# Performance work log

Measured on AMD Instinct MI355X. Metric: run time of the kernel, lower is better.

The kernel has to match this reference:

```python
import jax, jax.numpy as jnp
import numpy as np


def conv1d(x, w, b):
    # x: (N, Cin, W), w: (Cout, Cin, K) -> (N, Cout, W-K+1), VALID conv (torch Conv1d)
    y = jax.lax.conv_general_dilated(x, w, (1,), 'VALID', dimension_numbers=('NCH', 'OIH', 'NCH'))
    return y + b[None, :, None]


def cnn_block(x, w, b):
    # conv1d then MaxPool1d over the full valid length -> (N, Cout)
    return jnp.max(conv1d(x, w, b), axis=2)


def highway(x, Wp, bp, Wg, bg):
    p = jax.nn.relu(x @ Wp.T + bp)
    g = jax.nn.sigmoid(x @ Wg.T + bg)
    return g * p + (1.0 - g) * x


def lstm_masked(x, lens, Wih, Whh, bih, bhh):
    # x: (N, Wt, E); lens: (N,) valid lengths. Emulates pack_padded_sequence +
    # nn.LSTM + pad_packed_sequence: outputs are h_t for t < len, zeros after.
    N, Wt, _ = x.shape
    H = Whh.shape[1]
    bias = bih + bhh
    h0 = jnp.zeros((N, H), x.dtype)

    def step(carry, inp):
        xt, t = inp
        h, c = carry
        z = xt @ Wih.T + h @ Whh.T + bias  # (N, 4H), gate order i,f,g,o
        i, f, g, o = jnp.split(z, 4, axis=-1)
        c2 = jax.nn.sigmoid(f) * c + jax.nn.sigmoid(i) * jnp.tanh(g)
        h2 = jax.nn.sigmoid(o) * jnp.tanh(c2)
        valid = (t < lens)[:, None]
        h2 = jnp.where(valid, h2, h)
        c2 = jnp.where(valid, c2, c)
        return (h2, c2), jnp.where(valid, h2, jnp.zeros_like(h2))

    xs = jnp.moveaxis(x, 1, 0)  # (Wt, N, E)
    ts = jnp.arange(Wt)
    _, out = jax.lax.scan(step, (h0, h0), (xs, ts))
    return jnp.moveaxis(out, 0, 1)  # (N, Wt, H)


def setup_inputs() -> dict:
    key = jax.random.key(0)
    ks = jax.random.split(key, 32)
    B, T = 32, 48
    WL, WA, WE = 33, 50, 30
    EL, EA, EE, H = 300, 988, 20, 128
    CL, CA, CE = 128, 256, 64
    s = 0.02
    inp = {
        'x_lin': jax.random.normal(ks[0], (B, T, WL, EL), jnp.float32),
        'x_aco': jax.random.normal(ks[1], (B, T, WA, EA), jnp.float32),
        'x_emo': jax.random.normal(ks[2], (B, T, WE, EE), jnp.float32),
        'window_length': jax.random.randint(ks[3], (B, T), 0, WE).astype(jnp.int32) + 1,
        'length': jax.random.randint(ks[4], (B,), 1, T + 1).astype(jnp.int32),
        # CNN params
        'convL_w': s * jax.random.normal(ks[5], (CL, EL, 5), jnp.float32),
        'convL_b': jnp.zeros((CL,), jnp.float32),
        'convA_w': s * jax.random.normal(ks[6], (CA, EA, 10), jnp.float32),
        'convA_b': jnp.zeros((CA,), jnp.float32),
        'convE_w': s * jax.random.normal(ks[7], (CE, H, 3), jnp.float32),
        'convE_b': jnp.zeros((CE,), jnp.float32),
        # Highway params
        'hwL_Wp': s * jax.random.normal(ks[8], (CL, CL), jnp.float32),
        'hwL_bp': jnp.zeros((CL,), jnp.float32),
        'hwL_Wg': s * jax.random.normal(ks[9], (CL, CL), jnp.float32),
        'hwL_bg': jnp.zeros((CL,), jnp.float32),
        'hwA_Wp': s * jax.random.normal(ks[10], (CA, CA), jnp.float32),
        'hwA_bp': jnp.zeros((CA,), jnp.float32),
        'hwA_Wg': s * jax.random.normal(ks[11], (CA, CA), jnp.float32),
        'hwA_bg': jnp.zeros((CA,), jnp.float32),
        'hwE_Wp': s * jax.random.normal(ks[12], (CE, CE), jnp.float32),
        'hwE_bp': jnp.zeros((CE,), jnp.float32),
        'hwE_Wg': s * jax.random.normal(ks[13], (CE, CE), jnp.float32),
        'hwE_bg': jnp.zeros((CE,), jnp.float32),
        # LSTM params (nn.LSTM, 1 layer, batch_first)
        'lstm_Wih': s * jax.random.normal(ks[14], (4 * H, EE), jnp.float32),
        'lstm_Whh': s * jax.random.normal(ks[15], (4 * H, H), jnp.float32),
        'lstm_bih': jnp.zeros((4 * H,), jnp.float32),
        'lstm_bhh': jnp.zeros((4 * H,), jnp.float32),
    }
    return inp


def reference(x_lin, x_aco, x_emo, window_length, length,
              convL_w, convL_b, convA_w, convA_b, convE_w, convE_b,
              hwL_Wp, hwL_bp, hwL_Wg, hwL_bg,
              hwA_Wp, hwA_bp, hwA_Wg, hwA_bg,
              hwE_Wp, hwE_bp, hwE_Wg, hwE_bg,
              lstm_Wih, lstm_Whh, lstm_bih, lstm_bhh):
    B, T = x_lin.shape[:2]
    # Linguistic: per-window CNN + Highway (dropout = identity in eval)
    xl = x_lin.reshape(B * T, x_lin.shape[2], x_lin.shape[3]).transpose(0, 2, 1)  # (BT, 300, WL)
    outL = highway(cnn_block(xl, convL_w, convL_b), hwL_Wp, hwL_bp, hwL_Wg, hwL_bg)
    outL = outL.reshape(B, T, -1)
    # Acoustic
    xa = x_aco.reshape(B * T, x_aco.shape[2], x_aco.shape[3]).transpose(0, 2, 1)  # (BT, 988, WA)
    outA = highway(cnn_block(xa, convA_w, convA_b), hwA_Wp, hwA_bp, hwA_Wg, hwA_bg)
    outA = outA.reshape(B, T, -1)
    # Emotient: ragged per-window LSTM (packed semantics) -> CNN -> Highway
    xe = x_emo.reshape(B * T, x_emo.shape[2], x_emo.shape[3])  # (BT, WE, 20)
    lens = window_length.reshape(B * T)
    h = lstm_masked(xe, lens, lstm_Wih, lstm_Whh, lstm_bih, lstm_bhh)  # (BT, WE, 128)
    outE = highway(cnn_block(h.transpose(0, 2, 1), convE_w, convE_b), hwE_Wp, hwE_bp, hwE_Wg, hwE_bg)
    outE = outE.reshape(B, T, -1)
    # Concatenate modalities -> (B, T, 128+256+64) fed to the downstream head
    return jnp.concatenate([outL, outA, outE], axis=2)
```

## Files before the change

### kernel.cpp

```cpp
#include <hip/hip_runtime.h>
#include <hip/hip_bf16.h>
#include <math.h>

#define BTOT 1536
#define EL 300
#define ELP 320
#define WL_ 33
#define CL 128
#define LOUTL 29
#define KPL 1600
#define EA 988
#define EAP 992
#define WA_ 50
#define CA 256
#define LOUTA 41
#define KPA 9920
#define EE 20
#define WE_ 30
#define HH 128
#define CE 64
#define LOUTE 28
#define KPE 384
#define KDIML 1500
#define KDIMA 9880
#define KDIME 384

typedef __attribute__((ext_vector_type(4))) float f32x4;
typedef __attribute__((ext_vector_type(8))) short short8;

__device__ __forceinline__ unsigned short f2bf(float f) {
    unsigned int x = __float_as_uint(f);
    unsigned int r = (x + 0x7fffu + ((x >> 16) & 1u)) >> 16;
    return (unsigned short)r;
}

__device__ __forceinline__ float sigmf(float x) {
    return __builtin_amdgcn_rcpf(1.f + __expf(-x));
}
__device__ __forceinline__ float tanh_fast(float x) {
    return 1.f - 2.f * __builtin_amdgcn_rcpf(1.f + __expf(2.f * x));
}

#define GLD16(gp, lp) __builtin_amdgcn_global_load_lds( \
    (const __attribute__((address_space(1))) void*)(gp), \
    (__attribute__((address_space(3))) void*)(lp), 16, 0, 0)

template<int N> __device__ __forceinline__ void vmwait() {
    if constexpr (N == 0) asm volatile("s_waitcnt vmcnt(0)" ::: "memory");
    else if constexpr (N == 1) asm volatile("s_waitcnt vmcnt(1)" ::: "memory");
    else if constexpr (N == 2) asm volatile("s_waitcnt vmcnt(2)" ::: "memory");
    else if constexpr (N == 3) asm volatile("s_waitcnt vmcnt(3)" ::: "memory");
    else if constexpr (N == 4) asm volatile("s_waitcnt vmcnt(4)" ::: "memory");
    else if constexpr (N == 5) asm volatile("s_waitcnt vmcnt(5)" ::: "memory");
    else if constexpr (N == 6) asm volatile("s_waitcnt vmcnt(6)" ::: "memory");
    else if constexpr (N == 8) asm volatile("s_waitcnt vmcnt(8)" ::: "memory");
    else static_assert(N == 0, "add case");
}

__device__ __forceinline__ void tr_one(const float* a, float* at, int R, int C, int idx) {
    int r = idx / C, c = idx - r * C;
    at[c * R + r] = a[idx];
}
template<int CIN, int CINP, int KW, int COUT, int KPAD>
__device__ __forceinline__ void wt_one(const float* w, unsigned short* wt, int idx) {
    int co = idx / KPAD;
    int p  = idx - co * KPAD;
    int k  = p / CINP;
    int c  = p - k * CINP;
    float v = 0.f;
    if (k < KW && c < CIN) v = w[(co * CIN + c) * KW + k];
    wt[idx] = f2bf(v);
}
template<bool BIG>
__global__ void prep_all(const float* hwL_Wp, float* WpTL, const float* hwL_Wg, float* WgTL,
                         const float* hwA_Wp, float* WpTA, const float* hwA_Wg, float* WgTA,
                         const float* hwE_Wp, float* WpTE, const float* hwE_Wg, float* WgTE,
                         const float* lstm_Wih, float* WihT, const float* lstm_Whh, float* WhhT,
                         const float* convL_w, unsigned short* wtL,
                         const float* convE_w, unsigned short* wtE,
                         const float* convA_w, unsigned short* wtA,
                         unsigned short* whh_bf, unsigned short* wihp_bf) {
    constexpr int S1 = 16384, S2 = 16384, S3 = 65536, S4 = 65536, S5 = 4096, S6 = 4096;
    constexpr int S7 = 512 * 20, S8 = 512 * 128;
    constexpr int S9 = 128 * KPL, S10 = 64 * KPE, S11 = 512 * 128, S12 = 512 * 32;
    constexpr int S13 = CA * KPA;
    constexpr int SMALL = S1 + S2 + S3 + S4 + S5 + S6 + S7 + S8;
    constexpr int TOTAL = BIG ? (SMALL + S9 + S10 + S11 + S12 + S13) : SMALL;
    int stride = gridDim.x * blockDim.x;
    for (int i = blockIdx.x * blockDim.x + threadIdx.x; i < TOTAL; i += stride) {
        int idx = i;
        if (idx < S1) { tr_one(hwL_Wp, WpTL, 128, 128, idx); continue; } idx -= S1;
        if (idx < S2) { tr_one(hwL_Wg, WgTL, 128, 128, idx); continue; } idx -= S2;
        if (idx < S3) { tr_one(hwA_Wp, WpTA, 256, 256, idx); continue; } idx -= S3;
        if (idx < S4) { tr_one(hwA_Wg, WgTA, 256, 256, idx); continue; } idx -= S4;
        if (idx < S5) { tr_one(hwE_Wp, WpTE, 64, 64, idx); continue; } idx -= S5;
        if (idx < S6) { tr_one(hwE_Wg, WgTE, 64, 64, idx); continue; } idx -= S6;
        if (idx < S7) { tr_one(lstm_Wih, WihT, 512, 20, idx); continue; } idx -= S7;
        if (idx < S8) { tr_one(lstm_Whh, WhhT, 512, 128, idx); continue; } idx -= S8;
        if constexpr (BIG) {
            if (idx < S9) { wt_one<EL, ELP, 5, CL, KPL>(convL_w, wtL, idx); continue; } idx -= S9;
            if (idx < S10) { wt_one<HH, HH, 3, CE, KPE>(convE_w, wtE, idx); continue; } idx -= S10;
            if (idx < S11) { whh_bf[idx] = f2bf(lstm_Whh[idx]); continue; } idx -= S11;
            if (idx < S12) { int col = idx >> 5, e = idx & 31;
                             wihp_bf[idx] = (e < 20) ? f2bf(lstm_Wih[col * 20 + e]) : (unsigned short)0;
                             continue; } idx -= S12;
            wt_one<EA, EAP, 10, CA, KPA>(convA_w, wtA, idx);
        }
    }
}

template<int CIN, int CINP>
__device__ __forceinline__ void cvt_chunk(const float* in, unsigned short* out, int idx) {
    constexpr int CH = CINP / 8;
    int row = idx / CH, c0 = (idx - row * CH) * 8;
    const float* src = in + (size_t)row * CIN + c0;
    union { short8 s; unsigned short u[8]; } o;
    if (c0 + 8 <= CIN) {
        float4 v0 = *(const float4*)src;
        float4 v1 = *(const float4*)(src + 4);
        o.u[0]=f2bf(v0.x); o.u[1]=f2bf(v0.y); o.u[2]=f2bf(v0.z); o.u[3]=f2bf(v0.w);
        o.u[4]=f2bf(v1.x); o.u[5]=f2bf(v1.y); o.u[6]=f2bf(v1.z); o.u[7]=f2bf(v1.w);
    } else {
        #pragma unroll
        for (int j = 0; j < 8; ++j) o.u[j] = (c0 + j < CIN) ? f2bf(src[j]) : (unsigned short)0;
    }
    *(short8*)(out + (size_t)row * CINP + c0) = o.s;
}

#define LSTM_BLOCKS 96
#define CVTA_BLOCKS 1440

__global__ __launch_bounds__(512, 1)
void lstm_cvt(const float* __restrict__ x_emo,
              const unsigned short* __restrict__ wihp_bf, const unsigned short* __restrict__ whh_bf,
              const float* __restrict__ bih, const float* __restrict__ bhh,
              const int* __restrict__ lens, unsigned short* __restrict__ hbuf,
              const float* __restrict__ xa, unsigned short* __restrict__ outa)
{
    __shared__ __align__(16) unsigned short xq[WE_ * 16 * 32];
    __shared__ __align__(16) char h_s[2 * 16 * HH * 2];

    if (blockIdx.x >= LSTM_BLOCKS) {
        constexpr int NAC = (BTOT * WA_) * (EAP / 8);
        int stride = CVTA_BLOCKS * 512;
        for (int i = (blockIdx.x - LSTM_BLOCKS) * 512 + threadIdx.x; i < NAC; i += stride)
            cvt_chunk<EA, EAP>(xa, outa, i);
        return;
    }

    const int tid  = threadIdx.x;
    const int w    = tid >> 6;
    const int lane = tid & 63;
    const int lr   = lane & 15;
    const int lq   = lane >> 4;
    const int s0   = blockIdx.x * 16;
    const int c    = w * 16 + lr;

    short8 bfr[4][4];
    short8 bw[4];
    float bj[4];
    #pragma unroll
    for (int g = 0; g < 4; ++g) {
        int col = g * 128 + c;
        #pragma unroll
        for (int kt = 0; kt < 4; ++kt)
            bfr[g][kt] = *(const short8*)(whh_bf + (size_t)col * 128 + kt * 32 + lq * 8);
        bw[g] = *(const short8*)(wihp_bf + (size_t)col * 32 + lq * 8);
        bj[g] = bih[col] + bhh[col];
    }
    int len4[4];
    #pragma unroll
    for (int j = 0; j < 4; ++j) len4[j] = lens[s0 + lq * 4 + j];

    for (int i = tid; i < WE_ * 16 * 32; i += 512) {
        int t = i >> 9, r = (i >> 5) & 15, e = i & 31;
        xq[i] = (e < 20) ? f2bf(x_emo[(((size_t)(s0 + r) * WE_) + t) * 20 + e]) : (unsigned short)0;
    }
    for (int i = tid; i < 2048; i += 512) ((unsigned int*)h_s)[i] = 0u;

    float c_prev[4] = {0.f, 0.f, 0.f, 0.f};
    unsigned short hb_prev[4] = {0, 0, 0, 0};
    __syncthreads();

    for (int t = 0; t < WE_; ++t) {
        const char* hsr = h_s + (t & 1) * 4096;
        char* hsw = h_s + ((t & 1) ^ 1) * 4096;
        short8 ax = *(const short8*)((const char*)xq + (size_t)(t * 16 + lr) * 64 + lq * 16);
        short8 af[4];
        #pragma unroll
        for (int kt = 0; kt < 4; ++kt)
            af[kt] = *(const short8*)(hsr + ((lr * 256 + kt * 64 + lq * 16) ^ ((lr & 7) << 4)));
        f32x4 acc[4];
        #pragma unroll
        for (int g = 0; g < 4; ++g)
            acc[g] = __builtin_amdgcn_mfma_f32_16x16x32_bf16(ax, bw[g], (f32x4){0.f,0.f,0.f,0.f}, 0, 0, 0);
        #pragma unroll
        for (int kt = 0; kt < 4; ++kt)
            #pragma unroll
            for (int g = 0; g < 4; ++g)
                acc[g] = __builtin_amdgcn_mfma_f32_16x16x32_bf16(af[kt], bfr[g][kt], acc[g], 0, 0, 0);
        #pragma unroll
        for (int j = 0; j < 4; ++j) {
            int s = lq * 4 + j;
            float zi = acc[0][j] + bj[0];
            float zf = acc[1][j] + bj[1];
            float zg = acc[2][j] + bj[2];
            float zo = acc[3][j] + bj[3];
            float si = sigmf(zi), sf = sigmf(zf), so = sigmf(zo);
            float tg = tanh_fast(zg);
            float c2 = sf * c_prev[j] + si * tg;
            float h2 = so * tanh_fast(c2);
            bool valid = (t < len4[j]);
            c_prev[j] = valid ? c2 : c_prev[j];
            unsigned short h2b = f2bf(h2);
            unsigned short hn = valid ? h2b : hb_prev[j];
            hb_prev[j] = hn;
            *(unsigned short*)(hsw + (((s * HH + c) * 2) ^ ((s & 7) << 4))) = hn;
            hbuf[(((size_t)(s0 + s) * WE_) + t) * HH + c] = valid ? h2b : (unsigned short)0;
        }
        __syncthreads();
    }
}

#define CONVA_BLOCKS 768
#define CVTL_BLOCKS 512
__global__ __launch_bounds__(256, 2)
void conv_a_v11(const unsigned short* __restrict__ xb, const unsigned short* __restrict__ wt,
                const float* __restrict__ bias, float* __restrict__ pooled,
                const float* __restrict__ xl, unsigned short* __restrict__ outl)
{
    constexpr int LOUT = LOUTA, WIN = WA_, CINP = EAP, BN = 128, COUT = CA;
    constexpr int CCH  = CINP / 32;
    constexpr int KB   = CINP * 2;
    constexpr int KTOTB = CINP * 10 * 2;
    constexpr int ABUF = 4 * 64 * 64;
    constexpr int BBUF = BN * 64;
    constexpr int CPQ  = 96;

    __shared__ __align__(16) char smem[2 * ABUF + 5 * BBUF];

    if (blockIdx.x >= CONVA_BLOCKS) {
        constexpr int NLC = (BTOT * WL_) * (ELP / 8);
        int stride = CVTL_BLOCKS * 256;
        for (int i = (blockIdx.x - CONVA_BLOCKS) * 256 + threadIdx.x; i < NLC; i += stride)
            cvt_chunk<EL, ELP>(xl, outl, i);
        return;
    }

    const int tid  = threadIdx.x;
    const int lane = tid & 63;
    const int wid  = tid >> 6;
    const int lr   = lane & 15;
    const int lq   = lane >> 4;
    const int lq16 = lq * 16;

    int xcd = blockIdx.x & 7;
    int n = xcd & 1;
    int m = (xcd >> 1) * CPQ + (blockIdx.x >> 3);

    f32x4 acc[3][8];
    #pragma unroll
    for (int i = 0; i < 3; ++i)
        #pragma unroll
        for (int j = 0; j < 8; ++j) acc[i][j] = (f32x4){0.f, 0.f, 0.f, 0.f};

    const int aw_r = tid >> 2;
    const int aw   = (aw_r < WIN) ? aw_r : (WIN - 1);
    const int slot = tid & 3;
    const char* asrc[4];
    #pragma unroll
    for (int i = 0; i < 4; ++i)
        asrc[i] = (const char*)xb + ((size_t)((m * 4 + i) * WIN + aw)) * KB
                + ((slot * 16) ^ (((aw_r >> 1) & 3) << 4));
    const char* bsrc[2];
    #pragma unroll
    for (int i = 0; i < 2; ++i) {
        int col = (tid + i * 256) >> 2;
        bsrc[i] = (const char*)wt + (size_t)(n * BN + col) * KTOTB
                + ((slot * 16) ^ (((col >> 1) & 3) << 4));
    }

    char* const abuf0 = smem;
    char* const abuf1 = smem + ABUF;
    char* const bbase = smem + 2 * ABUF;

    int cbo[8];
    #pragma unroll
    for (int nf = 0; nf < 8; ++nf) {
        int cb = nf * 16 + lr;
        cbo[nf] = cb * 64 + (lq16 ^ (((cb >> 1) & 3) << 4));
    }

    #pragma unroll
    for (int i = 0; i < 4; ++i)
        GLD16(asrc[i], abuf0 + i * 4096 + tid * 16);
    #pragma unroll
    for (int s = 0; s < 3; ++s) {
        GLD16(bsrc[0] + s * KB, bbase + s * BBUF + tid * 16);
        GLD16(bsrc[1] + s * KB, bbase + s * BBUF + 4096 + tid * 16);
    }
    vmwait<0>();
    __builtin_amdgcn_s_barrier();

    int bcur = 0;

#define VSTEP(KK, DOA, DOBAR, WN, DOBSTG, CHN) do {                                \
    const char* bb = bbase + bcur * BBUF;                                          \
    short8 afr[3];                                                                 \
    _Pragma("unroll")                                                              \
    for (int o = 0; o < 3; ++o) {                                                  \
        int row = o * 16 + lr + (KK);                                              \
        afr[o] = *(const short8*)(awave + row * 64 + (lq16 ^ (((row >> 1) & 3) << 4))); \
    }                                                                              \
    short8 bf[8];                                                                  \
    _Pragma("unroll")                                                              \
    for (int nf = 0; nf < 8; ++nf) bf[nf] = *(const short8*)(bb + cbo[nf]);        \
    if (DOBSTG) {                                                                  \
        constexpr int K3 = ((KK) + 3 < 10) ? (KK) + 3 : (KK) - 7;                  \
        int boff = K3 * KB + (CHN) * 64;                                           \
        int b3 = bcur + 3; if (b3 >= 5) b3 -= 5;                                   \
        char* bstg = bbase + b3 * BBUF;                                            \
        GLD16(bsrc[0] + boff, bstg + tid * 16);                                    \
        GLD16(bsrc[1] + boff, bstg + 4096 + tid * 16);                             \
    }                                                                              \
    if (DOA) GLD16(asrc[(KK) - 5] + (size_t)(ci + 1) * 64,                         \
                   abn + ((KK) - 5) * 4096 + tid * 16);                            \
    __builtin_amdgcn_s_setprio(1);                                                 \
    _Pragma("unroll")                                                              \
    for (int nf = 0; nf < 8; ++nf)                                                 \
        _Pragma("unroll")                                                          \
        for (int o = 0; o < 3; ++o)                                                \
            acc[o][nf] = __builtin_amdgcn_mfma_f32_16x16x32_bf16(afr[o], bf[nf], acc[o][nf], 0, 0, 0); \
    __builtin_amdgcn_s_setprio(0);                                                 \
    if (DOBAR) { vmwait<WN>(); asm volatile("" ::: "memory");                      \
                 __builtin_amdgcn_s_barrier(); }                                   \
    bcur = (bcur == 4) ? 0 : bcur + 1;                                             \
} while (0)

    for (int ci = 0; ci < CCH - 1; ++ci) {
        const char* ab = (ci & 1) ? abuf1 : abuf0;
        char* abn = (ci & 1) ? abuf0 : abuf1;
        const char* awave = ab + wid * 4096;
        VSTEP(0, false, false, 0, true, ci);
        VSTEP(1, false, true,  2, true, ci);
        VSTEP(2, false, false, 0, true, ci);
        VSTEP(3, false, true,  2, true, ci);
        VSTEP(4, false, false, 0, true, ci);
        VSTEP(5, true,  true,  3, true, ci);
        VSTEP(6, true,  false, 0, true, ci);
        VSTEP(7, true,  true,  3, true, ci + 1);
        VSTEP(8, true,  false, 0, true, ci + 1);
        VSTEP(9, false, true,  2, true, ci + 1);
    }
    {
        const int ci = CCH - 1;
        const char* ab = (ci & 1) ? abuf1 : abuf0;
        char* abn = (ci & 1) ? abuf0 : abuf1; (void)abn;
        const char* awave = ab + wid * 4096;
        VSTEP(0, false, false, 0, true,  ci);
        VSTEP(1, false, true,  2, true,  ci);
        VSTEP(2, false, false, 0, true,  ci);
        VSTEP(3, false, true,  2, true,  ci);
        VSTEP(4, false, false, 0, true,  ci);
        VSTEP(5, false, true,  2, true,  ci);
        VSTEP(6, false, false, 0, true,  ci);
        VSTEP(7, false, true,  0, false, ci);
        VSTEP(8, false, false, 0, false, ci);
        VSTEP(9, false, true,  0, false, ci);
    }
#undef VSTEP

    const int bt = m * 4 + wid;
    #pragma unroll
    for (int nf = 0; nf < 8; ++nf) {
        float mx = -INFINITY;
        #pragma unroll
        for (int o = 0; o < 3; ++o) {
            int rb = o * 16 + lq * 4;
            #pragma unroll
            for (int j = 0; j < 4; ++j)
                if (rb + j < LOUT) mx = fmaxf(mx, acc[o][nf][j]);
        }
        mx = fmaxf(mx, __shfl_xor(mx, 16, 64));
        mx = fmaxf(mx, __shfl_xor(mx, 32, 64));
        if (lane < 16) {
            int col = n * BN + nf * 16 + lane;
            pooled[(size_t)bt * COUT + col] = mx + bias[col];
        }
    }
}

template<int LOUT, int WIN, int CINP, int KW, int BN, int NS, int MFR, int COUT>
__global__ __launch_bounds__(256, 2)
void conv_pool_v10(const unsigned short* __restrict__ xb, const unsigned short* __restrict__ wt,
                   const float* __restrict__ bias, float* __restrict__ pooled)
{
    constexpr int CCH   = CINP / 32;
    constexpr int KB    = CINP * 2;
    constexpr int KTOTB = CINP * KW * 2;
    constexpr int NFR   = BN / 16;
    constexpr int B_IT  = BN / 64;
    constexpr int ABUF  = 4 * 64 * 64;
    constexpr int BBUF  = BN * 64;
    constexpr int CPQ   = (BTOT / 4) / 4;

    __shared__ __align__(16) char smem[2 * ABUF + 4 * BBUF];

    const int tid  = threadIdx.x;
    const int lane = tid & 63;
    const int wid  = tid >> 6;
    const int lr   = lane & 15;
    const int lq   = lane >> 4;
    const int lq16 = lq * 16;

    int m, n;
    if constexpr (NS == 2) {
        int xcd = blockIdx.x & 7;
        n = xcd & 1;
        m = (xcd >> 1) * CPQ + (blockIdx.x >> 3);
    } else {
        m = blockIdx.x; n = 0;
    }

    f32x4 acc[MFR][NFR];
    #pragma unroll
    for (int i = 0; i < MFR; ++i)
        #pragma unroll
        for (int j = 0; j < NFR; ++j) acc[i][j] = (f32x4){0.f, 0.f, 0.f, 0.f};

    const int aw_r = tid >> 2;
    const int aw   = (aw_r < WIN) ? aw_r : (WIN - 1);
    const int slot = tid & 3;
    const char* asrc[4];
    #pragma unroll
    for (int i = 0; i < 4; ++i)
        asrc[i] = (const char*)xb + ((size_t)((m * 4 + i) * WIN + aw)) * KB
                + ((slot * 16) ^ (((aw_r >> 1) & 3) << 4));
    const char* bsrc[B_IT];
    #pragma unroll
    for (int i = 0; i < B_IT; ++i) {
        int col = (tid + i * 256) >> 2;
        bsrc[i] = (const char*)wt + (size_t)(n * BN + col) * KTOTB
                + ((slot * 16) ^ (((col >> 1) & 3) << 4));
    }

    char* const abuf0 = smem;
    char* const abuf1 = smem + ABUF;
    char* const bbase = smem + 2 * ABUF;

    int cbo[NFR];
    #pragma unroll
    for (int nf = 0; nf < NFR; ++nf) {
        int cb = nf * 16 + lr;
        cbo[nf] = cb * 64 + (lq16 ^ (((cb >> 1) & 3) << 4));
    }

    #pragma unroll
    for (int i = 0; i < 4; ++i)
        GLD16(asrc[i], abuf0 + i * 4096 + tid * 16);
    #pragma unroll
    for (int s = 0; s < 3; ++s)
        #pragma unroll
        for (int i = 0; i < B_IT; ++i)
            GLD16(bsrc[i] + s * KB, bbase + s * BBUF + i * 4096 + tid * 16);
    vmwait<0>();
    __builtin_amdgcn_s_barrier();

    int bcur = 0;

#define STEP(KK, WN, TAIL) do {                                                    \
    const char* bb = bbase + bcur * BBUF;                                          \
    short8 afr[MFR];                                                               \
    _Pragma("unroll")                                                              \
    for (int o = 0; o < MFR; ++o) {                                                \
        int row = o * 16 + lr + (KK);                                              \
        afr[o] = *(const short8*)(awave + row * 64 + (lq16 ^ (((row >> 1) & 3) << 4))); \
    }                                                                              \
    short8 bf[NFR];                                                                \
    _Pragma("unroll")                                                              \
    for (int nf = 0; nf < NFR; ++nf) bf[nf] = *(const short8*)(bb + cbo[nf]);      \
    if (!(TAIL) || (KK) < KW - 3) {                                                \
        constexpr int k3_ = ((KK) + 3 < KW) ? (KK) + 3 : (KK) + 3 - KW;            \
        int boff = k3_ * KB + (((KK) + 3 < KW) ? ci : ci + 1) * 64;                \
        char* bstg = bbase + ((bcur + 3) & 3) * BBUF;                              \
        _Pragma("unroll")                                                          \
        for (int i = 0; i < B_IT; ++i)                                             \
            GLD16(bsrc[i] + boff, bstg + i * 4096 + tid * 16);                     \
    }                                                                              \
    if (!(TAIL)) {                                                                 \
        if (KW >= 8) {                                                             \
            if ((KK) < 4)                                                          \
                GLD16(asrc[(KK) & 3] + (size_t)(ci + 1) * 64, abn + ((KK) & 3) * 4096 + tid * 16); \
        } else if ((KK) == 0) {                                                    \
            _Pragma("unroll")                                                      \
            for (int i = 0; i < 4; ++i)                                            \
                GLD16(asrc[i] + (size_t)(ci + 1) * 64, abn + i * 4096 + tid * 16); \
        }                                                                          \
    }                                                                              \
    __builtin_amdgcn_s_setprio(1);                                                 \
    _Pragma("unroll")                                                              \
    for (int nf = 0; nf < NFR; ++nf)                                               \
        _Pragma("unroll")                                                          \
        for (int o = 0; o < MFR; ++o)                                              \
            acc[o][nf] = __builtin_amdgcn_mfma_f32_16x16x32_bf16(afr[o], bf[nf], acc[o][nf], 0, 0, 0); \
    __builtin_amdgcn_s_setprio(0);                                                 \
    vmwait<WN>();                                                                  \
    asm volatile("" ::: "memory");                                                 \
    __builtin_amdgcn_s_barrier();                                                  \
    bcur = (bcur + 1) & 3;                                                         \
} while (0)

    for (int ci = 0; ci < CCH - 1; ++ci) {
        const char* ab = (ci & 1) ? abuf1 : abuf0;
        char* abn = (ci & 1) ? abuf0 : abuf1;
        const char* awave = ab + wid * 4096;
        if constexpr (KW == 5) {
            STEP(0, 8, false); STEP(1, 8, false); STEP(2, 4, false); STEP(3, 4, false); STEP(4, 4, false);
        } else {
            STEP(0, 6, false); STEP(1, 6, false); STEP(2, 2, false);
        }
    }
    {
        const int ci = CCH - 1;
        const char* ab = (ci & 1) ? abuf1 : abuf0;
        char* abn = (ci & 1) ? abuf0 : abuf1; (void)abn;
        const char* awave = ab + wid * 4096;
        if constexpr (KW == 5) {
            STEP(0, 4, true); STEP(1, 4, true); STEP(2, 2, true); STEP(3, 0, true); STEP(4, 0, true);
        } else {
            STEP(0, 1, true); STEP(1, 0, true); STEP(2, 0, true);
        }
    }
#undef STEP

    const int bt = m * 4 + wid;
    #pragma unroll
    for (int nf = 0; nf < NFR; ++nf) {
        float mx = -INFINITY;
        #pragma unroll
        for (int o = 0; o < MFR; ++o) {
            int rb = o * 16 + lq * 4;
            #pragma unroll
            for (int j = 0; j < 4; ++j)
                if (rb + j < LOUT) mx = fmaxf(mx, acc[o][nf][j]);
        }
        mx = fmaxf(mx, __shfl_xor(mx, 16, 64));
        mx = fmaxf(mx, __shfl_xor(mx, 32, 64));
        if (lane < 16) {
            int col = n * BN + nf * 16 + lane;
            pooled[(size_t)bt * COUT + col] = mx + bias[col];
        }
    }
}

#define HWA_BLOCKS 192
#define HWL_BLOCKS 96
#define HWE_BLOCKS 48
__global__ __launch_bounds__(256)
void highway_v2(const float* __restrict__ pL, const float* __restrict__ pA, const float* __restrict__ pE,
                const float* __restrict__ WpTL, const float* __restrict__ bpL,
                const float* __restrict__ WgTL, const float* __restrict__ bgL,
                const float* __restrict__ WpTA, const float* __restrict__ bpA,
                const float* __restrict__ WgTA, const float* __restrict__ bgA,
                const float* __restrict__ WpTE, const float* __restrict__ bpE,
                const float* __restrict__ WgTE, const float* __restrict__ bgE,
                float* __restrict__ out) {
    __shared__ float xs[2048];
    int bx = blockIdx.x;
    int tid = threadIdx.x;
    if (bx < HWA_BLOCKS) {
        int bt0 = bx * 8;
        #pragma unroll
        for (int s = 0; s < 8; ++s) xs[s * 256 + tid] = pA[(size_t)(bt0 + s) * 256 + tid];
        __syncthreads();
        float p[8], g[8];
        #pragma unroll
        for (int s = 0; s < 8; ++s) { p[s] = bpA[tid]; g[s] = bgA[tid]; }
        for (int c = 0; c < 256; ++c) {
            float wp = WpTA[c * 256 + tid], wg = WgTA[c * 256 + tid];
            #pragma unroll
            for (int s = 0; s < 8; ++s) {
                float xv = xs[s * 256 + c];
                p[s] += xv * wp; g[s] += xv * wg;
            }
        }
        #pragma unroll
        for (int s = 0; s < 8; ++s) {
            float pp = fmaxf(p[s], 0.f);
            float gg = sigmf(g[s]);
            out[(size_t)(bt0 + s) * 448 + 128 + tid] = gg * pp + (1.f - gg) * xs[s * 256 + tid];
        }
    } else if (bx < HWA_BLOCKS + HWL_BLOCKS) {
        int bt0 = (bx - HWA_BLOCKS) * 16;
        for (int i = tid; i < 16 * 128; i += 256) xs[i] = pL[(size_t)bt0 * 128 + i];
        __syncthreads();
        int j = tid & 127, h = tid >> 7;
        float p[8], g[8];
        #pragma unroll
        for (int s = 0; s < 8; ++s) { p[s] = bpL[j]; g[s] = bgL[j]; }
        for (int c = 0; c < 128; ++c) {
            float wp = WpTL[c * 128 + j], wg = WgTL[c * 128 + j];
            #pragma unroll
            for (int s = 0; s < 8; ++s) {
                float xv = xs[(h * 8 + s) * 128 + c];
                p[s] += xv * wp; g[s] += xv * wg;
            }
        }
        #pragma unroll
        for (int s = 0; s < 8; ++s) {
            float pp = fmaxf(p[s], 0.f);
            float gg = sigmf(g[s]);
            out[(size_t)(bt0 + h * 8 + s) * 448 + j] = gg * pp + (1.f - gg) * xs[(h * 8 + s) * 128 + j];
        }
    } else {
        int bt0 = (bx - HWA_BLOCKS - HWL_BLOCKS) * 32;
        for (int i = tid; i < 32 * 64; i += 256) xs[i] = pE[(size_t)bt0 * 64 + i];
        __syncthreads();
        int j = tid & 63, grp = tid >> 6;
        float p[8], g[8];
        #pragma unroll
        for (int s = 0; s < 8; ++s) { p[s] = bpE[j]; g[s] = bgE[j]; }
        for (int c = 0; c < 64; ++c) {
            float wp = WpTE[c * 64 + j], wg = WgTE[c * 64 + j];
            #pragma unroll
            for (int s = 0; s < 8; ++s) {
                float xv = xs[(grp * 8 + s) * 64 + c];
                p[s] += xv * wp; g[s] += xv * wg;
            }
        }
        #pragma unroll
        for (int s = 0; s < 8; ++s) {
            float pp = fmaxf(p[s], 0.f);
            float gg = sigmf(g[s]);
            out[(size_t)(bt0 + grp * 8 + s) * 448 + 384 + j] = gg * pp + (1.f - gg) * xs[(grp * 8 + s) * 64 + j];
        }
    }
}

__global__ __launch_bounds__(512)
void lstm_kernel_f32(const float* __restrict__ x, const int* __restrict__ lens,
                     const float* __restrict__ WihT, const float* __restrict__ WhhT,
                     const float* __restrict__ bih, const float* __restrict__ bhh,
                     float* __restrict__ hout) {
    int bt = blockIdx.x;
    int j  = threadIdx.x;
    __shared__ float xs[WE_][EE];
    __shared__ __align__(16) float hs[HH];
    __shared__ float zs[512];
    for (int idx = j; idx < WE_ * EE; idx += 512)
        ((float*)xs)[idx] = x[(size_t)bt * WE_ * EE + idx];
    if (j < HH) hs[j] = 0.f;
    float wih[EE];
    #pragma unroll
    for (int e = 0; e < EE; ++e) wih[e] = WihT[e * 512 + j];
    float whh[HH];
    #pragma unroll
    for (int h = 0; h < HH; ++h) whh[h] = WhhT[h * 512 + j];
    float bjv = bih[j] + bhh[j];
    float c_reg = 0.f;
    int len = lens[bt];
    __syncthreads();
    for (int t = 0; t < WE_; ++t) {
        float z = bjv;
        #pragma unroll
        for (int e = 0; e < EE; ++e) z += wih[e] * xs[t][e];
        const float4* h4 = (const float4*)hs;
        #pragma unroll
        for (int q = 0; q < HH / 4; ++q) {
            float4 hv = h4[q];
            z += whh[4*q+0] * hv.x + whh[4*q+1] * hv.y
               + whh[4*q+2] * hv.z + whh[4*q+3] * hv.w;
        }
        zs[j] = z;
        __syncthreads();
        if (j < HH) {
            float zi = zs[j], zf = zs[HH + j], zg = zs[2*HH + j], zo = zs[3*HH + j];
            float si = 1.f / (1.f + expf(-zi));
            float sf = 1.f / (1.f + expf(-zf));
            float so = 1.f / (1.f + expf(-zo));
            float tg = tanhf(zg);
            float c2 = sf * c_reg + si * tg;
            float h2 = so * tanhf(c2);
            bool valid = (t < len);
            float hn = valid ? h2 : hs[j];
            c_reg    = valid ? c2 : c_reg;
            hout[((size_t)bt * WE_ + t) * HH + j] = valid ? h2 : 0.f;
            hs[j] = hn;
        }
        __syncthreads();
    }
}

template<int CIN, int WIN, int COUT, int KDIM, int LOUT>
__global__ __launch_bounds__(256)
void conv_pool_simple(const float* __restrict__ x, const float* __restrict__ w,
                      const float* __restrict__ bias, float* __restrict__ pooled)
{
    constexpr int KW = KDIM / CIN;
    int bt = blockIdx.x;
    int co = blockIdx.y * 64 + (threadIdx.x & 63);
    int seg = threadIdx.x >> 6;
    __shared__ float part[4][64];
    float m = -INFINITY;
    for (int l = seg; l < LOUT; l += 4) {
        float acc = 0.f;
        for (int k = 0; k < KW; ++k) {
            const float* xr = x + ((size_t)bt * WIN + l + k) * CIN;
            const float* wr = w + ((size_t)co * CIN) * KW + k;
            for (int cc = 0; cc < CIN; ++cc) acc += xr[cc] * wr[(size_t)cc * KW];
        }
        m = fmaxf(m, acc);
    }
    part[seg][threadIdx.x & 63] = m;
    __syncthreads();
    if (threadIdx.x < 64) {
        float mm = fmaxf(fmaxf(part[0][threadIdx.x], part[1][threadIdx.x]),
                         fmaxf(part[2][threadIdx.x], part[3][threadIdx.x]));
        pooled[(size_t)bt * COUT + co] = mm + bias[co];
    }
}

static inline int cdiv(int a, int b) { return (a + b - 1) / b; }

extern "C" void kernel_launch(void* const* d_in, const int* in_sizes, int n_in,
                              void* d_out, int out_size, void* d_ws, size_t ws_size,
                              hipStream_t stream) {
    const float* x_lin  = (const float*)d_in[0];
    const float* x_aco  = (const float*)d_in[1];
    const float* x_emo  = (const float*)d_in[2];
    const int*   wlen   = (const int*)  d_in[3];
    const float* convL_w = (const float*)d_in[5];
    const float* convL_b = (const float*)d_in[6];
    const float* convA_w = (const float*)d_in[7];
    const float* convA_b = (const float*)d_in[8];
    const float* convE_w = (const float*)d_in[9];
    const float* convE_b = (const float*)d_in[10];
    const float* hwL_Wp = (const float*)d_in[11];
    const float* hwL_bp = (const float*)d_in[12];
    const float* hwL_Wg = (const float*)d_in[13];
    const float* hwL_bg = (const float*)d_in[14];
    const float* hwA_Wp = (const float*)d_in[15];
    const float* hwA_bp = (const float*)d_in[16];
    const float* hwA_Wg = (const float*)d_in[17];
    const float* hwA_bg = (const float*)d_in[18];
    const float* hwE_Wp = (const float*)d_in[19];
    const float* hwE_bp = (const float*)d_in[20];
    const float* hwE_Wg = (const float*)d_in[21];
    const float* hwE_bg = (const float*)d_in[22];
    const float* lstm_Wih = (const float*)d_in[23];
    const float* lstm_Whh = (const float*)d_in[24];
    const float* lstm_bih = (const float*)d_in[25];
    const float* lstm_bhh = (const float*)d_in[26];
    float* out = (float*)d_out;

    char* p0 = (char*)d_ws;
    char* p = p0;
    auto alloc = [&](size_t bytes) { char* r = p; p += (bytes + 255) & ~(size_t)255; return r; };
    float* WpTL = (float*)alloc((size_t)CL * CL * 4);
    float* WgTL = (float*)alloc((size_t)CL * CL * 4);
    float* WpTA = (float*)alloc((size_t)CA * CA * 4);
    float* WgTA = (float*)alloc((size_t)CA * CA * 4);
    float* WpTE = (float*)alloc((size_t)CE * CE * 4);
    float* WgTE = (float*)alloc((size_t)CE * CE * 4);
    float* WihT = (float*)alloc((size_t)EE * 512 * 4);
    float* WhhT = (float*)alloc((size_t)HH * 512 * 4);
    unsigned short* whh_bf  = (unsigned short*)alloc((size_t)512 * 128 * 2);
    unsigned short* wihp_bf = (unsigned short*)alloc((size_t)512 * 32 * 2);
    void*  hbuf = (void*)alloc((size_t)BTOT * WE_ * HH * 4);
    float* pL   = (float*)alloc((size_t)BTOT * CL * 4);
    float* pA   = (float*)alloc((size_t)BTOT * CA * 4);
    float* pE   = (float*)alloc((size_t)BTOT * CE * 4);
    unsigned short* wtA = (unsigned short*)alloc((size_t)CA * KPA * 2);
    unsigned short* wtL = (unsigned short*)alloc((size_t)CL * KPL * 2);
    unsigned short* wtE = (unsigned short*)alloc((size_t)CE * KPE * 2);
    unsigned short* xlin_p = (unsigned short*)alloc((size_t)BTOT * WL_ * ELP * 2 + 64);
    unsigned short* xaco_p = (unsigned short*)alloc((size_t)BTOT * WA_ * EAP * 2 + 64);
    size_t need = (size_t)(p - p0);
    bool big = ws_size >= need;

    if (big) {
        prep_all<true><<<2048, 256, 0, stream>>>(hwL_Wp, WpTL, hwL_Wg, WgTL, hwA_Wp, WpTA, hwA_Wg, WgTA,
                                                 hwE_Wp, WpTE, hwE_Wg, WgTE, lstm_Wih, WihT, lstm_Whh, WhhT,
                                                 convL_w, wtL, convE_w, wtE, convA_w, wtA, whh_bf, wihp_bf);
        lstm_cvt<<<LSTM_BLOCKS + CVTA_BLOCKS, 512, 0, stream>>>(
            x_emo, wihp_bf, whh_bf, lstm_bih, lstm_bhh, wlen, (unsigned short*)hbuf,
            x_aco, xaco_p);
        conv_a_v11<<<CONVA_BLOCKS + CVTL_BLOCKS, 256, 0, stream>>>(
            xaco_p, wtA, convA_b, pA, x_lin, xlin_p);
        conv_pool_v10<LOUTL, WL_, ELP, 5, 128, 1, 2, CL>
            <<<384, 256, 0, stream>>>(xlin_p, wtL, convL_b, pL);
        conv_pool_v10<LOUTE, WE_, HH, 3, 64, 1, 2, CE>
            <<<384, 256, 0, stream>>>((const unsigned short*)hbuf, wtE, convE_b, pE);
        highway_v2<<<HWA_BLOCKS + HWL_BLOCKS + HWE_BLOCKS, 256, 0, stream>>>(
            pL, pA, pE, WpTL, hwL_bp, WgTL, hwL_bg, WpTA, hwA_bp, WgTA, hwA_bg,
            WpTE, hwE_bp, WgTE, hwE_bg, out);
    } else {
        prep_all<false><<<2048, 256, 0, stream>>>(hwL_Wp, WpTL, hwL_Wg, WgTL, hwA_Wp, WpTA, hwA_Wg, WgTA,
                                                  hwE_Wp, WpTE, hwE_Wg, WgTE, lstm_Wih, WihT, lstm_Whh, WhhT,
                                                  convL_w, wtL, convE_w, wtE, convA_w, wtA, whh_bf, wihp_bf);
        lstm_kernel_f32<<<BTOT, 512, 0, stream>>>(x_emo, wlen, WihT, WhhT, lstm_bih, lstm_bhh, (float*)hbuf);
        conv_pool_simple<EA, WA_, CA, KDIMA, LOUTA>
            <<<dim3(BTOT, CA / 64), 256, 0, stream>>>(x_aco, convA_w, convA_b, pA);
        conv_pool_simple<EL, WL_, CL, KDIML, LOUTL>
            <<<dim3(BTOT, CL / 64), 256, 0, stream>>>(x_lin, convL_w, convL_b, pL);
        conv_pool_simple<HH, WE_, CE, KDIME, LOUTE>
            <<<dim3(BTOT, CE / 64), 256, 0, stream>>>((const float*)hbuf, convE_w, convE_b, pE);
        highway_v2<<<HWA_BLOCKS + HWL_BLOCKS + HWE_BLOCKS, 256, 0, stream>>>(
            pL, pA, pE, WpTL, hwL_bp, WgTL, hwL_bg, WpTA, hwA_bp, WgTA, hwA_bg,
            WpTE, hwE_bp, WgTE, hwE_bg, out);
    }
}
```

Baseline: 518.6 us.

## Merge three conv kernels into one launch and move x_lin conversion into LSTM kernel

The x_lin fp32-to-bf16 conversion moves from the conv_a kernel into the lstm_cvt kernel, sharing a grid-stride loop with the x_aco conversion. The conv_a, conv_L and conv_E kernels become device bodies dispatched by block index inside one conv_all launch of 1536 blocks, so the L and E convolutions can run alongside A instead of after it. This cuts launch count and tail idle time. In exchange every block reserves the largest shared-memory footprint (72 KB), which can lower occupancy for the L and E blocks.

```diff
diff --git a/kernel.cpp b/kernel.cpp
--- a/kernel.cpp
+++ b/kernel.cpp
@@ -51,7 +51,6 @@
     else if constexpr (N == 2) asm volatile("s_waitcnt vmcnt(2)" ::: "memory");
     else if constexpr (N == 3) asm volatile("s_waitcnt vmcnt(3)" ::: "memory");
     else if constexpr (N == 4) asm volatile("s_waitcnt vmcnt(4)" ::: "memory");
-    else if constexpr (N == 5) asm volatile("s_waitcnt vmcnt(5)" ::: "memory");
     else if constexpr (N == 6) asm volatile("s_waitcnt vmcnt(6)" ::: "memory");
     else if constexpr (N == 8) asm volatile("s_waitcnt vmcnt(8)" ::: "memory");
     else static_assert(N == 0, "add case");
@@ -71,6 +70,24 @@
     if (k < KW && c < CIN) v = w[(co * CIN + c) * KW + k];
     wt[idx] = f2bf(v);
 }
+template<int CIN, int CINP>
+__device__ __forceinline__ void cvt_chunk(const float* in, unsigned short* out, int idx) {
+    constexpr int CH = CINP / 8;
+    int row = idx / CH, c0 = (idx - row * CH) * 8;
+    const float* src = in + (size_t)row * CIN + c0;
+    union { short8 s; unsigned short u[8]; } o;
+    if (c0 + 8 <= CIN) {
+        float4 v0 = *(const float4*)src;
+        float4 v1 = *(const float4*)(src + 4);
+        o.u[0]=f2bf(v0.x); o.u[1]=f2bf(v0.y); o.u[2]=f2bf(v0.z); o.u[3]=f2bf(v0.w);
+        o.u[4]=f2bf(v1.x); o.u[5]=f2bf(v1.y); o.u[6]=f2bf(v1.z); o.u[7]=f2bf(v1.w);
+    } else {
+        #pragma unroll
+        for (int j = 0; j < 8; ++j) o.u[j] = (c0 + j < CIN) ? f2bf(src[j]) : (unsigned short)0;
+    }
+    *(short8*)(out + (size_t)row * CINP + c0) = o.s;
+}
+
 template<bool BIG>
 __global__ void prep_all(const float* hwL_Wp, float* WpTL, const float* hwL_Wg, float* WgTL,
                          const float* hwA_Wp, float* WpTA, const float* hwA_Wg, float* WgTA,
@@ -109,42 +126,28 @@
     }
 }
 
-template<int CIN, int CINP>
-__device__ __forceinline__ void cvt_chunk(const float* in, unsigned short* out, int idx) {
-    constexpr int CH = CINP / 8;
-    int row = idx / CH, c0 = (idx - row * CH) * 8;
-    const float* src = in + (size_t)row * CIN + c0;
-    union { short8 s; unsigned short u[8]; } o;
-    if (c0 + 8 <= CIN) {
-        float4 v0 = *(const float4*)src;
-        float4 v1 = *(const float4*)(src + 4);
-        o.u[0]=f2bf(v0.x); o.u[1]=f2bf(v0.y); o.u[2]=f2bf(v0.z); o.u[3]=f2bf(v0.w);
-        o.u[4]=f2bf(v1.x); o.u[5]=f2bf(v1.y); o.u[6]=f2bf(v1.z); o.u[7]=f2bf(v1.w);
-    } else {
-        #pragma unroll
-        for (int j = 0; j < 8; ++j) o.u[j] = (c0 + j < CIN) ? f2bf(src[j]) : (unsigned short)0;
-    }
-    *(short8*)(out + (size_t)row * CINP + c0) = o.s;
-}
-
 #define LSTM_BLOCKS 96
-#define CVTA_BLOCKS 1440
+#define CVT_BLOCKS 1952
 
 __global__ __launch_bounds__(512, 1)
 void lstm_cvt(const float* __restrict__ x_emo,
               const unsigned short* __restrict__ wihp_bf, const unsigned short* __restrict__ whh_bf,
               const float* __restrict__ bih, const float* __restrict__ bhh,
               const int* __restrict__ lens, unsigned short* __restrict__ hbuf,
-              const float* __restrict__ xa, unsigned short* __restrict__ outa)
+              const float* __restrict__ xa, const float* __restrict__ xl,
+              unsigned short* __restrict__ outa, unsigned short* __restrict__ outl)
 {
     __shared__ __align__(16) unsigned short xq[WE_ * 16 * 32];
     __shared__ __align__(16) char h_s[2 * 16 * HH * 2];
 
     if (blockIdx.x >= LSTM_BLOCKS) {
         constexpr int NAC = (BTOT * WA_) * (EAP / 8);
-        int stride = CVTA_BLOCKS * 512;
-        for (int i = (blockIdx.x - LSTM_BLOCKS) * 512 + threadIdx.x; i < NAC; i += stride)
-            cvt_chunk<EA, EAP>(xa, outa, i);
+        constexpr int NLC = (BTOT * WL_) * (ELP / 8);
+        int stride = CVT_BLOCKS * 512;
+        for (int i = (blockIdx.x - LSTM_BLOCKS) * 512 + threadIdx.x; i < NAC + NLC; i += stride) {
+            if (i < NAC) cvt_chunk<EA, EAP>(xa, outa, i);
+            else         cvt_chunk<EL, ELP>(xl, outl, i - NAC);
+        }
         return;
     }
 
@@ -222,12 +225,159 @@
     }
 }
 
-#define CONVA_BLOCKS 768
-#define CVTL_BLOCKS 512
-__global__ __launch_bounds__(256, 2)
-void conv_a_v11(const unsigned short* __restrict__ xb, const unsigned short* __restrict__ wt,
-                const float* __restrict__ bias, float* __restrict__ pooled,
-                const float* __restrict__ xl, unsigned short* __restrict__ outl)
+template<int LOUT, int WIN, int CINP, int KW, int BN, int MFR, int COUT>
+__device__ __forceinline__
+void conv_body_v10(char* smem, int m, int n,
+                   const unsigned short* __restrict__ xb, const unsigned short* __restrict__ wt,
+                   const float* __restrict__ bias, float* __restrict__ pooled)
+{
+    constexpr int CCH   = CINP / 32;
+    constexpr int KB    = CINP * 2;
+    constexpr int KTOTB = CINP * KW * 2;
+    constexpr int NFR   = BN / 16;
+    constexpr int B_IT  = BN / 64;
+    constexpr int ABUF  = 4 * 64 * 64;
+    constexpr int BBUF  = BN * 64;
+
+    const int tid  = threadIdx.x;
+    const int lane = tid & 63;
+    const int wid  = tid >> 6;
+    const int lr   = lane & 15;
+    const int lq   = lane >> 4;
+    const int lq16 = lq * 16;
+
+    f32x4 acc[MFR][NFR];
+    #pragma unroll
+    for (int i = 0; i < MFR; ++i)
+        #pragma unroll
+        for (int j = 0; j < NFR; ++j) acc[i][j] = (f32x4){0.f, 0.f, 0.f, 0.f};
+
+    const int aw_r = tid >> 2;
+    const int aw   = (aw_r < WIN) ? aw_r : (WIN - 1);
+    const int slot = tid & 3;
+    const char* asrc[4];
+    #pragma unroll
+    for (int i = 0; i < 4; ++i)
+        asrc[i] = (const char*)xb + ((size_t)((m * 4 + i) * WIN + aw)) * KB
+                + ((slot * 16) ^ (((aw_r >> 1) & 3) << 4));
+    const char* bsrc[B_IT];
+    #pragma unroll
+    for (int i = 0; i < B_IT; ++i) {
+        int col = (tid + i * 256) >> 2;
+        bsrc[i] = (const char*)wt + (size_t)(n * BN + col) * KTOTB
+                + ((slot * 16) ^ (((col >> 1) & 3) << 4));
+    }
+
+    char* const abuf0 = smem;
+    char* const abuf1 = smem + ABUF;
+    char* const bbase = smem + 2 * ABUF;
+
+    int cbo[NFR];
+    #pragma unroll
+    for (int nf = 0; nf < NFR; ++nf) {
+        int cb = nf * 16 + lr;
+        cbo[nf] = cb * 64 + (lq16 ^ (((cb >> 1) & 3) << 4));
+    }
+
+    #pragma unroll
+    for (int i = 0; i < 4; ++i)
+        GLD16(asrc[i], abuf0 + i * 4096 + tid * 16);
+    #pragma unroll
+    for (int s = 0; s < 3; ++s)
+        #pragma unroll
+        for (int i = 0; i < B_IT; ++i)
+            GLD16(bsrc[i] + s * KB, bbase + s * BBUF + i * 4096 + tid * 16);
+    vmwait<0>();
+    __builtin_amdgcn_s_barrier();
+
+    int bcur = 0;
+
+#define STEP(KK, WN, TAIL) do {                                                    \
+    const char* bb = bbase + bcur * BBUF;                                          \
+    short8 afr[MFR];                                                               \
+    _Pragma("unroll")                                                              \
+    for (int o = 0; o < MFR; ++o) {                                                \
+        int row = o * 16 + lr + (KK);                                              \
+        afr[o] = *(const short8*)(awave + row * 64 + (lq16 ^ (((row >> 1) & 3) << 4))); \
+    }                                                                              \
+    short8 bf[NFR];                                                                \
+    _Pragma("unroll")                                                              \
+    for (int nf = 0; nf < NFR; ++nf) bf[nf] = *(const short8*)(bb + cbo[nf]);      \
+    if (!(TAIL) || (KK) < KW - 3) {                                                \
+        constexpr int k3_ = ((KK) + 3 < KW) ? (KK) + 3 : (KK) + 3 - KW;            \
+        int boff = k3_ * KB + (((KK) + 3 < KW) ? ci : ci + 1) * 64;                \
+        char* bstg = bbase + ((bcur + 3) & 3) * BBUF;                              \
+        _Pragma("unroll")                                                          \
+        for (int i = 0; i < B_IT; ++i)                                             \
+            GLD16(bsrc[i] + boff, bstg + i * 4096 + tid * 16);                     \
+    }                                                                              \
+    if (!(TAIL)) {                                                                 \
+        if ((KK) == 0) {                                                           \
+            _Pragma("unroll")                                                      \
+            for (int i = 0; i < 4; ++i)                                            \
+                GLD16(asrc[i] + (size_t)(ci + 1) * 64, abn + i * 4096 + tid * 16); \
+        }                                                                          \
+    }                                                                              \
+    __builtin_amdgcn_s_setprio(1);                                                 \
+    _Pragma("unroll")                                                              \
+    for (int nf = 0; nf < NFR; ++nf)                                               \
+        _Pragma("unroll")                                                          \
+        for (int o = 0; o < MFR; ++o)                                              \
+            acc[o][nf] = __builtin_amdgcn_mfma_f32_16x16x32_bf16(afr[o], bf[nf], acc[o][nf], 0, 0, 0); \
+    __builtin_amdgcn_s_setprio(0);                                                 \
+    vmwait<WN>();                                                                  \
+    asm volatile("" ::: "memory");                                                 \
+    __builtin_amdgcn_s_barrier();                                                  \
+    bcur = (bcur + 1) & 3;                                                         \
+} while (0)
+
+    for (int ci = 0; ci < CCH - 1; ++ci) {
+        const char* ab = (ci & 1) ? abuf1 : abuf0;
+        char* abn = (ci & 1) ? abuf0 : abuf1;
+        const char* awave = ab + wid * 4096;
+        if constexpr (KW == 5) {
+            STEP(0, 8, false); STEP(1, 8, false); STEP(2, 4, false); STEP(3, 4, false); STEP(4, 4, false);
+        } else {
+            STEP(0, 6, false); STEP(1, 6, false); STEP(2, 2, false);
+        }
+    }
+    {
+        const int ci = CCH - 1;
+        const char* ab = (ci & 1) ? abuf1 : abuf0;
+        char* abn = (ci & 1) ? abuf0 : abuf1; (void)abn;
+        const char* awave = ab + wid * 4096;
+        if constexpr (KW == 5) {
+            STEP(0, 4, true); STEP(1, 4, true); STEP(2, 2, true); STEP(3, 0, true); STEP(4, 0, true);
+        } else {
+            STEP(0, 1, true); STEP(1, 0, true); STEP(2, 0, true);
+        }
+    }
+#undef STEP
+
+    const int bt = m * 4 + wid;
+    #pragma unroll
+    for (int nf = 0; nf < NFR; ++nf) {
+        float mx = -INFINITY;
+        #pragma unroll
+        for (int o = 0; o < MFR; ++o) {
+            int rb = o * 16 + lq * 4;
+            #pragma unroll
+            for (int j = 0; j < 4; ++j)
+                if (rb + j < LOUT) mx = fmaxf(mx, acc[o][nf][j]);
+        }
+        mx = fmaxf(mx, __shfl_xor(mx, 16, 64));
+        mx = fmaxf(mx, __shfl_xor(mx, 32, 64));
+        if (lane < 16) {
+            int col = n * BN + nf * 16 + lane;
+            pooled[(size_t)bt * COUT + col] = mx + bias[col];
+        }
+    }
+}
+
+__device__ __forceinline__
+void conv_body_a(char* smem, int m, int n,
+                 const unsigned short* __restrict__ xb, const unsigned short* __restrict__ wt,
+                 const float* __restrict__ bias, float* __restrict__ pooled)
 {
     constexpr int LOUT = LOUTA, WIN = WA_, CINP = EAP, BN = 128, COUT = CA;
     constexpr int CCH  = CINP / 32;
@@ -235,17 +385,6 @@
     constexpr int KTOTB = CINP * 10 * 2;
     constexpr int ABUF = 4 * 64 * 64;
     constexpr int BBUF = BN * 64;
-    constexpr int CPQ  = 96;
-
-    __shared__ __align__(16) char smem[2 * ABUF + 5 * BBUF];
-
-    if (blockIdx.x >= CONVA_BLOCKS) {
-        constexpr int NLC = (BTOT * WL_) * (ELP / 8);
-        int stride = CVTL_BLOCKS * 256;
-        for (int i = (blockIdx.x - CONVA_BLOCKS) * 256 + threadIdx.x; i < NLC; i += stride)
-            cvt_chunk<EL, ELP>(xl, outl, i);
-        return;
-    }
 
     const int tid  = threadIdx.x;
     const int lane = tid & 63;
@@ -253,10 +392,6 @@
     const int lr   = lane & 15;
     const int lq   = lane >> 4;
     const int lq16 = lq * 16;
-
-    int xcd = blockIdx.x & 7;
-    int n = xcd & 1;
-    int m = (xcd >> 1) * CPQ + (blockIdx.x >> 3);
 
     f32x4 acc[3][8];
     #pragma unroll
@@ -390,166 +525,29 @@
     }
 }
 
-template<int LOUT, int WIN, int CINP, int KW, int BN, int NS, int MFR, int COUT>
+#define CONVA_BLOCKS 768
+#define CONVL_BLOCKS 384
 __global__ __launch_bounds__(256, 2)
-void conv_pool_v10(const unsigned short* __restrict__ xb, const unsigned short* __restrict__ wt,
-                   const float* __restrict__ bias, float* __restrict__ pooled)
+void conv_all(const unsigned short* __restrict__ xaco_p, const unsigned short* __restrict__ wtA,
+              const float* __restrict__ convA_b, float* __restrict__ pA,
+              const unsigned short* __restrict__ xlin_p, const unsigned short* __restrict__ wtL,
+              const float* __restrict__ convL_b, float* __restrict__ pL,
+              const unsigned short* __restrict__ hbuf, const unsigned short* __restrict__ wtE,
+              const float* __restrict__ convE_b, float* __restrict__ pE)
 {
-    constexpr int CCH   = CINP / 32;
-    constexpr int KB    = CINP * 2;
-    constexpr int KTOTB = CINP * KW * 2;
-    constexpr int NFR   = BN / 16;
-    constexpr int B_IT  = BN / 64;
-    constexpr int ABUF  = 4 * 64 * 64;
-    constexpr int BBUF  = BN * 64;
-    constexpr int CPQ   = (BTOT / 4) / 4;
-
-    __shared__ __align__(16) char smem[2 * ABUF + 4 * BBUF];
-
-    const int tid  = threadIdx.x;
-    const int lane = tid & 63;
-    const int wid  = tid >> 6;
-    const int lr   = lane & 15;
-    const int lq   = lane >> 4;
-    const int lq16 = lq * 16;
-
-    int m, n;
-    if constexpr (NS == 2) {
-        int xcd = blockIdx.x & 7;
-        n = xcd & 1;
-        m = (xcd >> 1) * CPQ + (blockIdx.x >> 3);
+    __shared__ __align__(16) char smem[73728];
+    int bx = blockIdx.x;
+    if (bx < CONVA_BLOCKS) {
+        int xcd = bx & 7;
+        int n = xcd & 1;
+        int m = (xcd >> 1) * 96 + (bx >> 3);
+        conv_body_a(smem, m, n, xaco_p, wtA, convA_b, pA);
+    } else if (bx < CONVA_BLOCKS + CONVL_BLOCKS) {
+        conv_body_v10<LOUTL, WL_, ELP, 5, 128, 2, CL>(smem, bx - CONVA_BLOCKS, 0,
+                                                      xlin_p, wtL, convL_b, pL);
     } else {
-        m = blockIdx.x; n = 0;
-    }
-
-    f32x4 acc[MFR][NFR];
-    #pragma unroll
-    for (int i = 0; i < MFR; ++i)
-        #pragma unroll
-        for (int j = 0; j < NFR; ++j) acc[i][j] = (f32x4){0.f, 0.f, 0.f, 0.f};
-
-    const int aw_r = tid >> 2;
-    const int aw   = (aw_r < WIN) ? aw_r : (WIN - 1);
-    const int slot = tid & 3;
-    const char* asrc[4];
-    #pragma unroll
-    for (int i = 0; i < 4; ++i)
-        asrc[i] = (const char*)xb + ((size_t)((m * 4 + i) * WIN + aw)) * KB
-                + ((slot * 16) ^ (((aw_r >> 1) & 3) << 4));
-    const char* bsrc[B_IT];
-    #pragma unroll
-    for (int i = 0; i < B_IT; ++i) {
-        int col = (tid + i * 256) >> 2;
-        bsrc[i] = (const char*)wt + (size_t)(n * BN + col) * KTOTB
-                + ((slot * 16) ^ (((col >> 1) & 3) << 4));
-    }
-
-    char* const abuf0 = smem;
-    char* const abuf1 = smem + ABUF;
-    char* const bbase = smem + 2 * ABUF;
-
-    int cbo[NFR];
-    #pragma unroll
-    for (int nf = 0; nf < NFR; ++nf) {
-        int cb = nf * 16 + lr;
-        cbo[nf] = cb * 64 + (lq16 ^ (((cb >> 1) & 3) << 4));
-    }
-
-    #pragma unroll
-    for (int i = 0; i < 4; ++i)
-        GLD16(asrc[i], abuf0 + i * 4096 + tid * 16);
-    #pragma unroll
-    for (int s = 0; s < 3; ++s)
-        #pragma unroll
-        for (int i = 0; i < B_IT; ++i)
-            GLD16(bsrc[i] + s * KB, bbase + s * BBUF + i * 4096 + tid * 16);
-    vmwait<0>();
-    __builtin_amdgcn_s_barrier();
-
-    int bcur = 0;
-
-#define STEP(KK, WN, TAIL) do {                                                    \
-    const char* bb = bbase + bcur * BBUF;                                          \
-    short8 afr[MFR];                                                               \
-    _Pragma("unroll")                                                              \
-    for (int o = 0; o < MFR; ++o) {                                                \
-        int row = o * 16 + lr + (KK);                                              \
-        afr[o] = *(const short8*)(awave + row * 64 + (lq16 ^ (((row >> 1) & 3) << 4))); \
-    }                                                                              \
-    short8 bf[NFR];                                                                \
-    _Pragma("unroll")                                                              \
-    for (int nf = 0; nf < NFR; ++nf) bf[nf] = *(const short8*)(bb + cbo[nf]);      \
-    if (!(TAIL) || (KK) < KW - 3) {                                                \
-        constexpr int k3_ = ((KK) + 3 < KW) ? (KK) + 3 : (KK) + 3 - KW;            \
-        int boff = k3_ * KB + (((KK) + 3 < KW) ? ci : ci + 1) * 64;                \
-        char* bstg = bbase + ((bcur + 3) & 3) * BBUF;                              \
-        _Pragma("unroll")                                                          \
-        for (int i = 0; i < B_IT; ++i)                                             \
-            GLD16(bsrc[i] + boff, bstg + i * 4096 + tid * 16);                     \
-    }                                                                              \
-    if (!(TAIL)) {                                                                 \
-        if (KW >= 8) {                                                             \
-            if ((KK) < 4)                                                          \
-                GLD16(asrc[(KK) & 3] + (size_t)(ci + 1) * 64, abn + ((KK) & 3) * 4096 + tid * 16); \
-        } else if ((KK) == 0) {                                                    \
-            _Pragma("unroll")                                                      \
-            for (int i = 0; i < 4; ++i)                                            \
-                GLD16(asrc[i] + (size_t)(ci + 1) * 64, abn + i * 4096 + tid * 16); \
-        }                                                                          \
-    }                                                                              \
-    __builtin_amdgcn_s_setprio(1);                                                 \
-    _Pragma("unroll")                                                              \
-    for (int nf = 0; nf < NFR; ++nf)                                               \
-        _Pragma("unroll")                                                          \
-        for (int o = 0; o < MFR; ++o)                                              \
-            acc[o][nf] = __builtin_amdgcn_mfma_f32_16x16x32_bf16(afr[o], bf[nf], acc[o][nf], 0, 0, 0); \
-    __builtin_amdgcn_s_setprio(0);                                                 \
-    vmwait<WN>();                                                                  \
-    asm volatile("" ::: "memory");                                                 \
-    __builtin_amdgcn_s_barrier();                                                  \
-    bcur = (bcur + 1) & 3;                                                         \
-} while (0)
-
-    for (int ci = 0; ci < CCH - 1; ++ci) {
-        const char* ab = (ci & 1) ? abuf1 : abuf0;
-        char* abn = (ci & 1) ? abuf0 : abuf1;
-        const char* awave = ab + wid * 4096;
-        if constexpr (KW == 5) {
-            STEP(0, 8, false); STEP(1, 8, false); STEP(2, 4, false); STEP(3, 4, false); STEP(4, 4, false);
-        } else {
-            STEP(0, 6, false); STEP(1, 6, false); STEP(2, 2, false);
-        }
-    }
-    {
-        const int ci = CCH - 1;
-        const char* ab = (ci & 1) ? abuf1 : abuf0;
-        char* abn = (ci & 1) ? abuf0 : abuf1; (void)abn;
-        const char* awave = ab + wid * 4096;
-        if constexpr (KW == 5) {
-            STEP(0, 4, true); STEP(1, 4, true); STEP(2, 2, true); STEP(3, 0, true); STEP(4, 0, true);
-        } else {
-            STEP(0, 1, true); STEP(1, 0, true); STEP(2, 0, true);
-        }
-    }
-#undef STEP
-
-    const int bt = m * 4 + wid;
-    #pragma unroll
-    for (int nf = 0; nf < NFR; ++nf) {
-        float mx = -INFINITY;
-        #pragma unroll
-        for (int o = 0; o < MFR; ++o) {
-            int rb = o * 16 + lq * 4;
-            #pragma unroll
-            for (int j = 0; j < 4; ++j)
-                if (rb + j < LOUT) mx = fmaxf(mx, acc[o][nf][j]);
-        }
-        mx = fmaxf(mx, __shfl_xor(mx, 16, 64));
-        mx = fmaxf(mx, __shfl_xor(mx, 32, 64));
-        if (lane < 16) {
-            int col = n * BN + nf * 16 + lane;
-            pooled[(size_t)bt * COUT + col] = mx + bias[col];
-        }
+        conv_body_v10<LOUTE, WE_, HH, 3, 64, 2, CE>(smem, bx - CONVA_BLOCKS - CONVL_BLOCKS, 0,
+                                                    hbuf, wtE, convE_b, pE);
     }
 }
 
@@ -782,15 +780,12 @@
         prep_all<true><<<2048, 256, 0, stream>>>(hwL_Wp, WpTL, hwL_Wg, WgTL, hwA_Wp, WpTA, hwA_Wg, WgTA,
                                                  hwE_Wp, WpTE, hwE_Wg, WgTE, lstm_Wih, WihT, lstm_Whh, WhhT,
                                                  convL_w, wtL, convE_w, wtE, convA_w, wtA, whh_bf, wihp_bf);
-        lstm_cvt<<<LSTM_BLOCKS + CVTA_BLOCKS, 512, 0, stream>>>(
+        lstm_cvt<<<LSTM_BLOCKS + CVT_BLOCKS, 512, 0, stream>>>(
             x_emo, wihp_bf, whh_bf, lstm_bih, lstm_bhh, wlen, (unsigned short*)hbuf,
-            x_aco, xaco_p);
-        conv_a_v11<<<CONVA_BLOCKS + CVTL_BLOCKS, 256, 0, stream>>>(
-            xaco_p, wtA, convA_b, pA, x_lin, xlin_p);
-        conv_pool_v10<LOUTL, WL_, ELP, 5, 128, 1, 2, CL>
-            <<<384, 256, 0, stream>>>(xlin_p, wtL, convL_b, pL);
-        conv_pool_v10<LOUTE, WE_, HH, 3, 64, 1, 2, CE>
-            <<<384, 256, 0, stream>>>((const unsigned short*)hbuf, wtE, convE_b, pE);
+            x_aco, x_lin, xaco_p, xlin_p);
+        conv_all<<<1536, 256, 0, stream>>>(xaco_p, wtA, convA_b, pA,
+                                           xlin_p, wtL, convL_b, pL,
+                                           (const unsigned short*)hbuf, wtE, convE_b, pE);
         highway_v2<<<HWA_BLOCKS + HWL_BLOCKS + HWE_BLOCKS, 256, 0, stream>>>(
             pL, pA, pE, WpTL, hwL_bp, WgTL, hwL_bg, WpTA, hwA_bp, WgTA, hwA_bg,
             WpTE, hwE_bp, WgTE, hwE_bg, out);
```

Result: slower. 535.1 us (+3.2%).
